# Performance work log

Hardware: AMD Instinct MI355X
Metric: run time of the kernel (lower is better)

Reference implementation:

```python
import jax, jax.numpy as jnp
import numpy as np

EMBED_DIM = 128
HIDDEN_DIM = 32
BN_EPS = 1e-5


def setup_inputs() -> dict:
    key = jax.random.key(0)
    ks = jax.random.split(key, 11)
    B, N, D, H = 16, 2048, EMBED_DIM, HIDDEN_DIM
    s_d = 1.0 / np.sqrt(D)
    return {
        "f_in": jax.random.normal(ks[0], (B, N, D), dtype=jnp.float32),
        "w_q": jax.random.uniform(ks[1], (H, D), jnp.float32, -s_d, s_d),
        "b_q": jax.random.uniform(ks[2], (H,), jnp.float32, -s_d, s_d),
        "w_k": jax.random.uniform(ks[3], (H, D), jnp.float32, -s_d, s_d),
        "b_k": jax.random.uniform(ks[4], (H,), jnp.float32, -s_d, s_d),
        "w_v": jax.random.uniform(ks[5], (D, D), jnp.float32, -s_d, s_d),
        "b_v": jax.random.uniform(ks[6], (D,), jnp.float32, -s_d, s_d),
        "w_l": jax.random.uniform(ks[7], (D, D), jnp.float32, -s_d, s_d),
        "b_l": jax.random.uniform(ks[8], (D,), jnp.float32, -s_d, s_d),
        "bn_gamma": jnp.ones((D,), jnp.float32),
        "bn_beta": jnp.zeros((D,), jnp.float32),
    }


def reference(f_in, w_q, b_q, w_k, b_k, w_v, b_v, w_l, b_l, bn_gamma, bn_beta):
    # Q/K/V projections: (B, N, D) -> (B, N, h) / (B, N, D)
    q = jnp.einsum("bnd,hd->bnh", f_in, w_q) + b_q
    k = jnp.einsum("bnd,hd->bnh", f_in, w_k) + b_k
    v = jnp.einsum("bnd,ed->bne", f_in, w_v) + b_v
    # scores (B, N, N); softmax over dim=1 (query axis), then L1-renorm over keys
    a = jnp.einsum("bnh,bmh->bnm", q, k)
    a = jax.nn.softmax(a, axis=1)
    a = a / jnp.sum(a, axis=2, keepdims=True)
    f_sa = jnp.einsum("bnm,bme->bne", a, v)
    # LBR: Linear -> BatchNorm (training stats over B and N) -> ReLU, residual add
    x = f_in - f_sa
    y = jnp.einsum("bnd,ed->bne", x, w_l) + b_l
    mean = jnp.mean(y, axis=(0, 1))
    var = jnp.var(y, axis=(0, 1))  # biased, as BatchNorm uses for normalization
    y = bn_gamma * (y - mean) * jax.lax.rsqrt(var + BN_EPS) + bn_beta
    return jax.nn.relu(y) + f_sa
```

## Files before the change

### kernel.cpp

```cpp
#include <hip/hip_runtime.h>
#include <stdint.h>

#define NB 16
#define NN 2048
#define ND 128
#define NH 32
#define NS (NB*NN)
#define NT 32

typedef __attribute__((ext_vector_type(8))) short bf16x8;
typedef __attribute__((ext_vector_type(4))) float f32x4;
typedef __attribute__((ext_vector_type(16))) float f32x16;

__device__ __forceinline__ unsigned short f2bf(float f){
  union { float f; unsigned int u; } v; v.f = f;
  unsigned int r = v.u + 0x7fffu + ((v.u >> 16) & 1u);
  return (unsigned short)(r >> 16);
}
__device__ __forceinline__ float bf2f(unsigned short u){
  union { unsigned int u; float f; } v; v.u = ((unsigned int)u) << 16;
  return v.f;
}
__device__ __forceinline__ float fexp2(float x){
  float r; asm("v_exp_f32 %0, %1" : "=v"(r) : "v"(x)); return r;
}

__global__ __launch_bounds__(256) void k_prep(const float* wq, const float* wk, const float* wv, const float* wl,
                                              unsigned short* oq, unsigned short* ok, unsigned short* ov, unsigned short* ol){
  int i = blockIdx.x*256 + threadIdx.x;
  if (i < 4096) oq[i] = f2bf(wq[i]);
  else if (i < 8192) ok[i-4096] = f2bf(wk[i-4096]);
  else if (i < 24576) ov[i-8192] = f2bf(wv[i-8192]);
  else if (i < 40960) ol[i-24576] = f2bf(wl[i-24576]);
}

__global__ __launch_bounds__(256) void k_qkv(const float* f, const unsigned short* wbq, const unsigned short* wbk,
                                             const unsigned short* wbv, const float* bq, const float* bk, const float* bv,
                                             unsigned short* Qb, unsigned short* Kb, unsigned short* Vb){
  int tid = threadIdx.x, wave = tid>>6, lane = tid&63, lr = lane&15, lg = lane>>4;
  long r0 = (long)blockIdx.x*64 + wave*16;
  bf16x8 a[4];
  const float* frow = f + (r0 + lr)*ND;
  #pragma unroll
  for (int ks=0; ks<4; ks++){
    const float* p = frow + ks*32 + lg*8;
    bf16x8 t;
    #pragma unroll
    for (int j=0;j<8;j++) t[j] = (short)f2bf(p[j]);
    a[ks] = t;
  }
  #pragma unroll
  for (int cs=0; cs<12; cs++){
    const unsigned short* wsrc; const float* bsrc; int cl;
    if (cs<2){ wsrc=wbq; bsrc=bq; cl=cs*16; }
    else if (cs<4){ wsrc=wbk; bsrc=bk; cl=(cs-2)*16; }
    else { wsrc=wbv; bsrc=bv; cl=(cs-4)*16; }
    f32x4 acc = {0.f,0.f,0.f,0.f};
    #pragma unroll
    for (int ks=0;ks<4;ks++){
      bf16x8 b = *(const bf16x8*)(wsrc + (cl+lr)*ND + ks*32 + lg*8);
      acc = __builtin_amdgcn_mfma_f32_16x16x32_bf16(a[ks], b, acc, 0, 0, 0);
    }
    float bias = bsrc[cl + lr];
    #pragma unroll
    for (int r=0;r<4;r++){
      float v = acc[r] + bias;
      if (cs<2) v *= 1.4426950408889634f;
      long row = r0 + lg*4 + r;
      if (cs<2) Qb[row*NH + cl+lr] = f2bf(v);
      else if (cs<4) Kb[row*NH + cl+lr] = f2bf(v);
      else Vb[row*ND + cl+lr] = f2bf(v);
    }
  }
}

__global__ __launch_bounds__(256) void k_csv(const unsigned short* Qb, const unsigned short* Kb,
                                             const unsigned short* Vb, unsigned short* VT){
  __shared__ unsigned short tr[128][65];
  __shared__ float wsh[64];
  int tid=threadIdx.x, wave=tid>>6, lane=tid&63, lr=lane&15, lg=lane>>4;
  int wg = (blockIdx.x & 7)*64 + (blockIdx.x >> 3);
  int b = wg >> 5;
  int m0 = (wg & 31)*64;
  const unsigned short* Qbb = Qb + (long)b*NN*NH;
  const unsigned short* Kbb = Kb + (long)b*NN*NH;
  const unsigned short* Vbb = Vb + ((long)b*NN + m0)*ND;
  bf16x8 vreg[4];
  #pragma unroll
  for (int it=0; it<4; it++){
    int i = it*256 + tid;
    int r = i >> 4, c8 = (i & 15)*8;
    vreg[it] = *(const bf16x8*)(Vbb + r*ND + c8);
  }
  bf16x8 kf = *(const bf16x8*)(Kbb + (m0 + wave*16 + lr)*NH + lg*8);
  float csum = 0.f;
  for (int n0=0; n0<NN; n0+=64){
    #pragma unroll
    for (int u=0; u<4; u++){
      bf16x8 qf = *(const bf16x8*)(Qbb + (n0+u*16+lr)*NH + lg*8);
      f32x4 c = {0.f,0.f,0.f,0.f};
      c = __builtin_amdgcn_mfma_f32_16x16x32_bf16(qf, kf, c, 0, 0, 0);
      csum += fexp2(c[0]) + fexp2(c[1]) + fexp2(c[2]) + fexp2(c[3]);
    }
  }
  csum += __shfl_xor(csum, 16, 64);
  csum += __shfl_xor(csum, 32, 64);
  #pragma unroll
  for (int it=0; it<4; it++){
    int i = it*256 + tid;
    int r = i >> 4, c8 = (i & 15)*8;
    #pragma unroll
    for (int j=0;j<8;j++) tr[c8+j][r] = (unsigned short)vreg[it][j];
  }
  if (lg == 0) wsh[wave*16 + lr] = 1.f / csum;
  __syncthreads();
  unsigned short* VTb = VT + (long)b*160*NN;
  #pragma unroll
  for (int it=0; it<9; it++){
    int i = it*256 + tid;
    int e = i >> 4, m4 = (i & 15)*4;
    ushort4 o;
    if (e < 128){
      o.x = f2bf(bf2f(tr[e][m4+0]) * wsh[m4+0]);
      o.y = f2bf(bf2f(tr[e][m4+1]) * wsh[m4+1]);
      o.z = f2bf(bf2f(tr[e][m4+2]) * wsh[m4+2]);
      o.w = f2bf(bf2f(tr[e][m4+3]) * wsh[m4+3]);
    } else if (e == 128){
      o.x = f2bf(wsh[m4+0]); o.y = f2bf(wsh[m4+1]);
      o.z = f2bf(wsh[m4+2]); o.w = f2bf(wsh[m4+3]);
    } else { o.x = o.y = o.z = o.w = 0; }
    *(ushort4*)(VTb + (long)e*NN + m0 + m4) = o;
  }
  {
    int e = 144 + (tid >> 4), m4 = (tid & 15)*4;
    ushort4 z; z.x = z.y = z.z = z.w = 0;
    *(ushort4*)(VTb + (long)e*NN + m0 + m4) = z;
  }
}

__global__ __launch_bounds__(128) void k_pv(const unsigned short* Qb, const unsigned short* Kb,
                                            const unsigned short* VT, unsigned short* fsab){
  __shared__ __align__(16) unsigned char vts[3][20480];
  int tid=threadIdx.x, wave=tid>>6, lane=tid&63;
  int l31 = lane & 31, H = lane >> 5;
  int wg = (blockIdx.x & 7)*64 + (blockIdx.x >> 3);
  int b = wg >> 5;
  int q0 = (wg & 31)*64 + wave*32;
  const unsigned short* Qbb = Qb + (long)b*NN*NH;
  const unsigned short* Kbb = Kb + (long)b*NN*NH;
  const unsigned short* VTb = VT + (long)b*160*NN;

  auto stageV = [&](int buf, int m0c){
    #pragma unroll
    for (int t=0;t<10;t++){
      int i = wave*10 + t;
      int e = i*8 + (lane>>3);
      int sblk = (lane&7) ^ (e&7);
      __builtin_amdgcn_global_load_lds(
        (const __attribute__((address_space(1))) unsigned int*)(VTb + (long)e*NN + m0c + sblk*8),
        (__attribute__((address_space(3))) unsigned int*)(&vts[buf][i*1024]), 16, 0, 0);
    }
  };

  bf16x8 qf0 = *(const bf16x8*)(Qbb + (long)(q0 + l31)*NH + 8*H);
  bf16x8 qf1 = *(const bf16x8*)(Qbb + (long)(q0 + l31)*NH + 16 + 8*H);
  asm volatile("" ::: "memory");
  bf16x8 k00 = *(const bf16x8*)(Kbb + (long)(l31)*NH + 8*H);
  bf16x8 k01 = *(const bf16x8*)(Kbb + (long)(l31)*NH + 16 + 8*H);
  bf16x8 k10 = *(const bf16x8*)(Kbb + (long)(32 + l31)*NH + 8*H);
  bf16x8 k11 = *(const bf16x8*)(Kbb + (long)(32 + l31)*NH + 16 + 8*H);
  asm volatile("" ::: "memory");
  stageV(0, 0);
  stageV(1, 64);

  f32x16 acc[5];
  #pragma unroll
  for (int c=0;c<5;c++)
    #pragma unroll
    for (int r=0;r<16;r++) acc[c][r] = 0.f;

  union U { unsigned int u[4]; bf16x8 v; };

  int vc = 0, vs = 2;
  for (int it = 0; it < NT; ++it){
    if (it == 0)         asm volatile("s_waitcnt vmcnt(10)" ::: "memory");
    else if (it == 1)    asm volatile("s_waitcnt vmcnt(14)" ::: "memory");
    else if (it == NT-1) asm volatile("s_waitcnt vmcnt(8)"  ::: "memory");
    else                 asm volatile("s_waitcnt vmcnt(18)" ::: "memory");
    __builtin_amdgcn_s_barrier();
    if (it + 2 < NT) stageV(vs, (it+2)*64);
    asm volatile("" ::: "memory");
    const unsigned char* vcur = &vts[vc][0];

    #pragma unroll
    for (int t=0;t<2;t++){
      f32x16 s;
      #pragma unroll
      for (int r=0;r<16;r++) s[r] = 0.f;
      s = __builtin_amdgcn_mfma_f32_32x32x16_bf16(t ? k10 : k00, qf0, s, 0, 0, 0);
      s = __builtin_amdgcn_mfma_f32_32x32x16_bf16(t ? k11 : k01, qf1, s, 0, 0, 0);
      #pragma unroll
      for (int r=0;r<16;r++) s[r] = fexp2(s[r]);
      unsigned int pk[8], sw[8];
      #pragma unroll
      for (int p=0;p<8;p++){
        asm("v_cvt_pk_bf16_f32 %0, %1, %2" : "=v"(pk[p]) : "v"(s[2*p]), "v"(s[2*p+1]));
        sw[p] = (unsigned int)__shfl_xor((int)pk[p], 32, 64);
      }
      bool h0 = (H == 0);
      U fa0, fa1;
      fa0.u[0] = h0 ? pk[0] : sw[2];  fa0.u[1] = h0 ? pk[1] : sw[3];
      fa0.u[2] = h0 ? sw[0] : pk[2];  fa0.u[3] = h0 ? sw[1] : pk[3];
      fa1.u[0] = h0 ? pk[4] : sw[6];  fa1.u[1] = h0 ? pk[5] : sw[7];
      fa1.u[2] = h0 ? sw[4] : pk[6];  fa1.u[3] = h0 ? sw[5] : pk[7];
      __builtin_amdgcn_s_setprio(1);
      #pragma unroll
      for (int ksl=0; ksl<2; ksl++){
        int KS = 2*t + ksl;
        const U& fa = ksl ? fa1 : fa0;
        #pragma unroll
        for (int c=0;c<5;c++){
          int e = c*32 + l31;
          bf16x8 vb = *(const bf16x8*)(vcur + (e<<7) + (((2*KS + H) ^ (e&7))<<4));
          acc[c] = __builtin_amdgcn_mfma_f32_32x32x16_bf16(fa.v, vb, acc[c], 0, 0, 0);
        }
      }
      __builtin_amdgcn_s_setprio(0);
    }
    if (it + 1 < NT){
      long mb = (long)(it+1)*64;
      k00 = *(const bf16x8*)(Kbb + (mb + l31)*NH + 8*H);
      k01 = *(const bf16x8*)(Kbb + (mb + l31)*NH + 16 + 8*H);
      k10 = *(const bf16x8*)(Kbb + (mb + 32 + l31)*NH + 8*H);
      k11 = *(const bf16x8*)(Kbb + (mb + 32 + l31)*NH + 16 + 8*H);
    }
    vc = (vc==2)?0:vc+1;
    vs = (vs==2)?0:vs+1;
  }
  long rowbase = (long)b*NN + q0;
  #pragma unroll
  for (int r=0;r<16;r++){
    float den = __shfl(acc[4][r], lane & 32, 64);
    float rinv = 1.f / den;
    int rho = (r&3) + 8*(r>>2) + 4*H;
    long row = rowbase + rho;
    #pragma unroll
    for (int c=0;c<4;c++)
      fsab[row*ND + c*32 + l31] = f2bf(acc[c][r] * rinv);
  }
}

__global__ __launch_bounds__(256) void k_lin(const float* f, const unsigned short* fsab, const unsigned short* wbl, const float* bl,
                                             unsigned short* ybuf, float* part){
  __shared__ float psum[4][128], psq[4][128];
  int tid=threadIdx.x, wave=tid>>6, lane=tid&63, lr=lane&15, lg=lane>>4;
  long r0 = (long)blockIdx.x*64 + wave*16;
  bf16x8 a[4];
  {
    const float* fr = f + (r0+lr)*ND;
    const unsigned short* sr = fsab + (r0+lr)*ND;
    #pragma unroll
    for (int ks=0;ks<4;ks++){
      bf16x8 sv = *(const bf16x8*)(sr + ks*32 + lg*8);
      bf16x8 t;
      #pragma unroll
      for (int j=0;j<8;j++){
        int d = ks*32 + lg*8 + j;
        t[j] = (short)f2bf(fr[d] - bf2f((unsigned short)sv[j]));
      }
      a[ks] = t;
    }
  }
  #pragma unroll
  for (int cs=0;cs<8;cs++){
    f32x4 acc = {0.f,0.f,0.f,0.f};
    #pragma unroll
    for (int ks=0;ks<4;ks++){
      bf16x8 bfr = *(const bf16x8*)(wbl + (cs*16+lr)*ND + ks*32 + lg*8);
      acc = __builtin_amdgcn_mfma_f32_16x16x32_bf16(a[ks], bfr, acc, 0, 0, 0);
    }
    float bias = bl[cs*16+lr];
    float l1=0.f, l2=0.f;
    #pragma unroll
    for (int r=0;r<4;r++){
      float y = acc[r] + bias;
      ybuf[(r0 + lg*4 + r)*ND + cs*16 + lr] = f2bf(y);
      l1 += y; l2 += y*y;
    }
    l1 += __shfl_xor(l1,16,64); l1 += __shfl_xor(l1,32,64);
    l2 += __shfl_xor(l2,16,64); l2 += __shfl_xor(l2,32,64);
    if (lg==0){ psum[wave][cs*16+lr] = l1; psq[wave][cs*16+lr] = l2; }
  }
  __syncthreads();
  if (tid < 128){
    float t1 = psum[0][tid]+psum[1][tid]+psum[2][tid]+psum[3][tid];
    float t2 = psq[0][tid]+psq[1][tid]+psq[2][tid]+psq[3][tid];
    part[tid*512 + blockIdx.x] = t1;
    part[65536 + tid*512 + blockIdx.x] = t2;
  }
}

__global__ __launch_bounds__(64) void k_bnred(const float* part, const float* gamma, const float* beta, float* bnstat){
  int c = blockIdx.x, t = threadIdx.x;
  float s=0.f, q=0.f;
  for (int i=t; i<512; i+=64){ s += part[c*512+i]; q += part[65536 + c*512+i]; }
  #pragma unroll
  for (int m=1; m<64; m<<=1){ s += __shfl_xor(s,m,64); q += __shfl_xor(q,m,64); }
  if (t==0){
    float mean = s * (1.f/(float)NS);
    float var  = q * (1.f/(float)NS) - mean*mean;
    float rstd = rsqrtf(var + 1e-5f);
    float sc = gamma[c]*rstd;
    bnstat[c] = sc;
    bnstat[128+c] = beta[c] - mean*sc;
  }
}

__global__ __launch_bounds__(256) void k_final(const unsigned short* ybuf, const unsigned short* fsab, const float* bnstat,
                                               float* out){
  long i0 = ((long)blockIdx.x*256 + threadIdx.x)*8;
  int c0 = (int)(i0 & (ND-1));
  bf16x8 yv = *(const bf16x8*)(ybuf + i0);
  bf16x8 fv = *(const bf16x8*)(fsab + i0);
  f32x4 o0, o1;
  #pragma unroll
  for (int j=0;j<8;j++){
    int c = c0 + j;
    float v = bf2f((unsigned short)yv[j]) * bnstat[c] + bnstat[128+c];
    v = v > 0.f ? v : 0.f;
    float r = v + bf2f((unsigned short)fv[j]);
    if (j<4) o0[j] = r; else o1[j-4] = r;
  }
  *(f32x4*)(out + i0) = o0;
  *(f32x4*)(out + i0 + 4) = o1;
}

extern "C" void kernel_launch(void* const* d_in, const int* in_sizes, int n_in,
                              void* d_out, int out_size, void* d_ws, size_t ws_size,
                              hipStream_t stream){
  const float* f_in  = (const float*)d_in[0];
  const float* w_q   = (const float*)d_in[1];
  const float* b_q   = (const float*)d_in[2];
  const float* w_k   = (const float*)d_in[3];
  const float* b_k   = (const float*)d_in[4];
  const float* w_v   = (const float*)d_in[5];
  const float* b_v   = (const float*)d_in[6];
  const float* w_l   = (const float*)d_in[7];
  const float* b_l   = (const float*)d_in[8];
  const float* gamma = (const float*)d_in[9];
  const float* beta  = (const float*)d_in[10];
  float* out = (float*)d_out;
  char* ws = (char*)d_ws;

  unsigned short* wbq = (unsigned short*)(ws + 0);
  unsigned short* wbk = (unsigned short*)(ws + 8192);
  unsigned short* wbv = (unsigned short*)(ws + 16384);
  unsigned short* wbl = (unsigned short*)(ws + 49152);
  unsigned short* Qb  = (unsigned short*)(ws + 81920);
  unsigned short* Kb  = (unsigned short*)(ws + 2179072);
  unsigned short* Vb  = (unsigned short*)(ws + 4276224);
  unsigned short* VT  = (unsigned short*)(ws + 12795904);
  unsigned short* fsab= (unsigned short*)(ws + 23281664);
  unsigned short* ybuf= (unsigned short*)(ws + 39010304);
  float*          part= (float*)(ws + 47398912);
  float*          bnst= (float*)(ws + 47923200);

  k_prep  <<<160, 256, 0, stream>>>(w_q, w_k, w_v, w_l, wbq, wbk, wbv, wbl);
  k_qkv   <<<512, 256, 0, stream>>>(f_in, wbq, wbk, wbv, b_q, b_k, b_v, Qb, Kb, Vb);
  k_csv   <<<512, 256, 0, stream>>>(Qb, Kb, Vb, VT);
  k_pv    <<<512, 128, 0, stream>>>(Qb, Kb, VT, fsab);
  k_lin   <<<512, 256, 0, stream>>>(f_in, fsab, wbl, b_l, ybuf, part);
  k_bnred <<<128, 64, 0, stream>>>(part, gamma, beta, bnst);
  k_final <<<2048,256, 0, stream>>>(ybuf, fsab, bnst, out);
}
```

Measured before the change: 132.5 us.

## Split attention key range across block halves and combine partials in new kernel

After: 115.9 us. 12.5% less time.

```diff
diff --git a/kernel.cpp b/kernel.cpp
--- a/kernel.cpp
+++ b/kernel.cpp
@@ -6,11 +6,11 @@
 #define ND 128
 #define NH 32
 #define NS (NB*NN)
-#define NT 32
 
 typedef __attribute__((ext_vector_type(8))) short bf16x8;
 typedef __attribute__((ext_vector_type(4))) float f32x4;
 typedef __attribute__((ext_vector_type(16))) float f32x16;
+typedef __attribute__((ext_vector_type(2))) int i32x2;
 
 __device__ __forceinline__ unsigned short f2bf(float f){
   union { float f; unsigned int u; } v; v.f = f;
@@ -23,6 +23,19 @@
 }
 __device__ __forceinline__ float fexp2(float x){
   float r; asm("v_exp_f32 %0, %1" : "=v"(r) : "v"(x)); return r;
+}
+__device__ __forceinline__ void pswap(unsigned int &x, unsigned int &y){
+#if __has_builtin(__builtin_amdgcn_permlane32_swap)
+  i32x2 r = __builtin_amdgcn_permlane32_swap((int)x, (int)y, false, false);
+  x = (unsigned int)r[0]; y = (unsigned int)r[1];
+#else
+  unsigned int sx = (unsigned int)__shfl_xor((int)x, 32, 64);
+  unsigned int sy = (unsigned int)__shfl_xor((int)y, 32, 64);
+  bool hi = ((threadIdx.x & 63) >> 5) != 0;
+  unsigned int nx = hi ? sy : x;
+  unsigned int ny = hi ? y  : sx;
+  x = nx; y = ny;
+#endif
 }
 
 __global__ __launch_bounds__(256) void k_prep(const float* wq, const float* wk, const float* wv, const float* wl,
@@ -138,22 +151,26 @@
   }
 }
 
-__global__ __launch_bounds__(128) void k_pv(const unsigned short* Qb, const unsigned short* Kb,
-                                            const unsigned short* VT, unsigned short* fsab){
+__global__ __launch_bounds__(256) void k_pv(const unsigned short* Qb, const unsigned short* Kb,
+                                            const unsigned short* VT, unsigned short* pnum, float* pden){
   __shared__ __align__(16) unsigned char vts[3][20480];
   int tid=threadIdx.x, wave=tid>>6, lane=tid&63;
   int l31 = lane & 31, H = lane >> 5;
   int wg = (blockIdx.x & 7)*64 + (blockIdx.x >> 3);
-  int b = wg >> 5;
-  int q0 = (wg & 31)*64 + wave*32;
+  int half = wg & 1;
+  int bq = wg >> 1;
+  int b = bq >> 4;
+  int q0 = (bq & 15)*128 + wave*32;
+  int mbase = half*1024;
+  const int NT2 = 16;
   const unsigned short* Qbb = Qb + (long)b*NN*NH;
   const unsigned short* Kbb = Kb + (long)b*NN*NH;
   const unsigned short* VTb = VT + (long)b*160*NN;
 
   auto stageV = [&](int buf, int m0c){
     #pragma unroll
-    for (int t=0;t<10;t++){
-      int i = wave*10 + t;
+    for (int t=0;t<5;t++){
+      int i = wave*5 + t;
       int e = i*8 + (lane>>3);
       int sblk = (lane&7) ^ (e&7);
       __builtin_amdgcn_global_load_lds(
@@ -164,14 +181,15 @@
 
   bf16x8 qf0 = *(const bf16x8*)(Qbb + (long)(q0 + l31)*NH + 8*H);
   bf16x8 qf1 = *(const bf16x8*)(Qbb + (long)(q0 + l31)*NH + 16 + 8*H);
+  bf16x8 k00 = *(const bf16x8*)(Kbb + (long)(mbase + l31)*NH + 8*H);
+  bf16x8 k01 = *(const bf16x8*)(Kbb + (long)(mbase + l31)*NH + 16 + 8*H);
+  bf16x8 k10 = *(const bf16x8*)(Kbb + (long)(mbase + 32 + l31)*NH + 8*H);
+  bf16x8 k11 = *(const bf16x8*)(Kbb + (long)(mbase + 32 + l31)*NH + 16 + 8*H);
   asm volatile("" ::: "memory");
-  bf16x8 k00 = *(const bf16x8*)(Kbb + (long)(l31)*NH + 8*H);
-  bf16x8 k01 = *(const bf16x8*)(Kbb + (long)(l31)*NH + 16 + 8*H);
-  bf16x8 k10 = *(const bf16x8*)(Kbb + (long)(32 + l31)*NH + 8*H);
-  bf16x8 k11 = *(const bf16x8*)(Kbb + (long)(32 + l31)*NH + 16 + 8*H);
+  stageV(0, mbase);
   asm volatile("" ::: "memory");
-  stageV(0, 0);
-  stageV(1, 64);
+  stageV(1, mbase + 64);
+  asm volatile("" ::: "memory");
 
   f32x16 acc[5];
   #pragma unroll
@@ -182,13 +200,22 @@
   union U { unsigned int u[4]; bf16x8 v; };
 
   int vc = 0, vs = 2;
-  for (int it = 0; it < NT; ++it){
-    if (it == 0)         asm volatile("s_waitcnt vmcnt(10)" ::: "memory");
-    else if (it == 1)    asm volatile("s_waitcnt vmcnt(14)" ::: "memory");
-    else if (it == NT-1) asm volatile("s_waitcnt vmcnt(8)"  ::: "memory");
-    else                 asm volatile("s_waitcnt vmcnt(18)" ::: "memory");
+  for (int it = 0; it < NT2; ++it){
+    if (it == 0)        asm volatile("s_waitcnt vmcnt(5)" ::: "memory");
+    else if (it < NT2-1) asm volatile("s_waitcnt vmcnt(9)" ::: "memory");
+    else                asm volatile("s_waitcnt vmcnt(0)" ::: "memory");
     __builtin_amdgcn_s_barrier();
-    if (it + 2 < NT) stageV(vs, (it+2)*64);
+    bf16x8 n00, n01, n10, n11;
+    bool pf = (it + 1 < NT2);
+    if (pf){
+      long mb = mbase + (long)(it+1)*64;
+      n00 = *(const bf16x8*)(Kbb + (mb + l31)*NH + 8*H);
+      n01 = *(const bf16x8*)(Kbb + (mb + l31)*NH + 16 + 8*H);
+      n10 = *(const bf16x8*)(Kbb + (mb + 32 + l31)*NH + 8*H);
+      n11 = *(const bf16x8*)(Kbb + (mb + 32 + l31)*NH + 16 + 8*H);
+    }
+    asm volatile("" ::: "memory");
+    if (it + 2 < NT2) stageV(vs, mbase + (it+2)*64);
     asm volatile("" ::: "memory");
     const unsigned char* vcur = &vts[vc][0];
 
@@ -201,18 +228,17 @@
       s = __builtin_amdgcn_mfma_f32_32x32x16_bf16(t ? k11 : k01, qf1, s, 0, 0, 0);
       #pragma unroll
       for (int r=0;r<16;r++) s[r] = fexp2(s[r]);
-      unsigned int pk[8], sw[8];
+      unsigned int pk[8];
       #pragma unroll
-      for (int p=0;p<8;p++){
+      for (int p=0;p<8;p++)
         asm("v_cvt_pk_bf16_f32 %0, %1, %2" : "=v"(pk[p]) : "v"(s[2*p]), "v"(s[2*p+1]));
-        sw[p] = (unsigned int)__shfl_xor((int)pk[p], 32, 64);
-      }
-      bool h0 = (H == 0);
+      pswap(pk[0], pk[2]);
+      pswap(pk[1], pk[3]);
+      pswap(pk[4], pk[6]);
+      pswap(pk[5], pk[7]);
       U fa0, fa1;
-      fa0.u[0] = h0 ? pk[0] : sw[2];  fa0.u[1] = h0 ? pk[1] : sw[3];
-      fa0.u[2] = h0 ? sw[0] : pk[2];  fa0.u[3] = h0 ? sw[1] : pk[3];
-      fa1.u[0] = h0 ? pk[4] : sw[6];  fa1.u[1] = h0 ? pk[5] : sw[7];
-      fa1.u[2] = h0 ? sw[4] : pk[6];  fa1.u[3] = h0 ? sw[5] : pk[7];
+      fa0.u[0] = pk[0]; fa0.u[1] = pk[1]; fa0.u[2] = pk[2]; fa0.u[3] = pk[3];
+      fa1.u[0] = pk[4]; fa1.u[1] = pk[5]; fa1.u[2] = pk[6]; fa1.u[3] = pk[7];
       __builtin_amdgcn_s_setprio(1);
       #pragma unroll
       for (int ksl=0; ksl<2; ksl++){
@@ -227,27 +253,34 @@
       }
       __builtin_amdgcn_s_setprio(0);
     }
-    if (it + 1 < NT){
-      long mb = (long)(it+1)*64;
-      k00 = *(const bf16x8*)(Kbb + (mb + l31)*NH + 8*H);
-      k01 = *(const bf16x8*)(Kbb + (mb + l31)*NH + 16 + 8*H);
-      k10 = *(const bf16x8*)(Kbb + (mb + 32 + l31)*NH + 8*H);
-      k11 = *(const bf16x8*)(Kbb + (mb + 32 + l31)*NH + 16 + 8*H);
-    }
+    if (pf){ k00 = n00; k01 = n01; k10 = n10; k11 = n11; }
     vc = (vc==2)?0:vc+1;
     vs = (vs==2)?0:vs+1;
   }
-  long rowbase = (long)b*NN + q0;
+  unsigned short* pn = pnum + (long)half*NS*ND + (long)b*NN*ND;
+  float* pd = pden + (long)half*NS + (long)b*NN;
   #pragma unroll
   for (int r=0;r<16;r++){
-    float den = __shfl(acc[4][r], lane & 32, 64);
-    float rinv = 1.f / den;
     int rho = (r&3) + 8*(r>>2) + 4*H;
-    long row = rowbase + rho;
+    long q = q0 + rho;
     #pragma unroll
     for (int c=0;c<4;c++)
-      fsab[row*ND + c*32 + l31] = f2bf(acc[c][r] * rinv);
-  }
+      pn[q*ND + c*32 + l31] = f2bf(acc[c][r]);
+    if (l31 == 0) pd[q] = acc[4][r];
+  }
+}
+
+__global__ __launch_bounds__(256) void k_comb(const unsigned short* pnum, const float* pden, unsigned short* fsab){
+  long i0 = ((long)blockIdx.x*256 + threadIdx.x)*8;
+  long q = i0 >> 7;
+  float rinv = 1.f / (pden[q] + pden[NS + q]);
+  bf16x8 a = *(const bf16x8*)(pnum + i0);
+  bf16x8 bb = *(const bf16x8*)(pnum + (long)NS*ND + i0);
+  bf16x8 o;
+  #pragma unroll
+  for (int j=0;j<8;j++)
+    o[j] = (short)f2bf((bf2f((unsigned short)a[j]) + bf2f((unsigned short)bb[j])) * rinv);
+  *(bf16x8*)(fsab + i0) = o;
 }
 
 __global__ __launch_bounds__(256) void k_lin(const float* f, const unsigned short* fsab, const unsigned short* wbl, const float* bl,
@@ -358,17 +391,20 @@
   unsigned short* wbl = (unsigned short*)(ws + 49152);
   unsigned short* Qb  = (unsigned short*)(ws + 81920);
   unsigned short* Kb  = (unsigned short*)(ws + 2179072);
-  unsigned short* Vb  = (unsigned short*)(ws + 4276224);
-  unsigned short* VT  = (unsigned short*)(ws + 12795904);
-  unsigned short* fsab= (unsigned short*)(ws + 23281664);
-  unsigned short* ybuf= (unsigned short*)(ws + 39010304);
-  float*          part= (float*)(ws + 47398912);
-  float*          bnst= (float*)(ws + 47923200);
+  unsigned short* VT  = (unsigned short*)(ws + 4276224);
+  unsigned short* Vb  = (unsigned short*)(ws + 14761984);
+  unsigned short* fsab= (unsigned short*)(ws + 14761984);
+  unsigned short* pnum= (unsigned short*)(ws + 23150592);
+  unsigned short* ybuf= (unsigned short*)(ws + 23150592);
+  float*          part= (float*)(ws + 31539200);
+  float*          pden= (float*)(ws + 39927808);
+  float*          bnst= (float*)(ws + 40189952);
 
   k_prep  <<<160, 256, 0, stream>>>(w_q, w_k, w_v, w_l, wbq, wbk, wbv, wbl);
   k_qkv   <<<512, 256, 0, stream>>>(f_in, wbq, wbk, wbv, b_q, b_k, b_v, Qb, Kb, Vb);
   k_csv   <<<512, 256, 0, stream>>>(Qb, Kb, Vb, VT);
-  k_pv    <<<512, 128, 0, stream>>>(Qb, Kb, VT, fsab);
+  k_pv    <<<512, 256, 0, stream>>>(Qb, Kb, VT, pnum, pden);
+  k_comb  <<<2048,256, 0, stream>>>(pnum, pden, fsab);
   k_lin   <<<512, 256, 0, stream>>>(f_in, fsab, wbl, b_l, ybuf, part);
   k_bnred <<<128, 64, 0, stream>>>(part, gamma, beta, bnst);
   k_final <<<2048,256, 0, stream>>>(ybuf, fsab, bnst, out);
```
